# Kernel tuning notes

Measured on AMD Instinct MI355X. Metric: run time of the kernel, lower is better.

Reference implementation:

```python
import jax, jax.numpy as jnp
import numpy as np

N, C = 50000, 256
H, D = 8, 64          # num_heads, out_channels (per-head dim)
M = 64                # nb_random_features
EPS = 1e-6


def _create_projection_matrix(m, d, seed=0):
    """Performer orthogonal random features: stacked orthogonal blocks scaled by chi-norms."""
    rng = np.random.RandomState(seed)
    blocks = []
    nb_full = m // d
    for _ in range(nb_full):
        q, _ = np.linalg.qr(rng.randn(d, d))
        blocks.append(q.T)
    rem = m - nb_full * d
    if rem > 0:
        q, _ = np.linalg.qr(rng.randn(d, d))
        blocks.append(q.T[:rem])
    multiplier = np.linalg.norm(rng.randn(m, d), axis=1)  # scaling == 0 path
    return (multiplier[:, None] * np.vstack(blocks)).astype(np.float32)


def setup_inputs() -> dict:
    key = jax.random.key(0)
    ks = jax.random.split(key, 9)
    s = 0.05  # small init so exp() of random features stays well-conditioned
    return {
        "x":     jax.random.normal(ks[0], (N, C), dtype=jnp.float32),
        "Wq_w":  jax.random.normal(ks[1], (C, H * D), dtype=jnp.float32) * s,
        "Wq_b":  jnp.zeros((H * D,), dtype=jnp.float32),
        "Wk_w":  jax.random.normal(ks[2], (C, H * D), dtype=jnp.float32) * s,
        "Wk_b":  jnp.zeros((H * D,), dtype=jnp.float32),
        "Wv_w":  jax.random.normal(ks[3], (C, H * D), dtype=jnp.float32) * s,
        "Wv_b":  jnp.zeros((H * D,), dtype=jnp.float32),
        "Wo_w":  jax.random.normal(ks[4], (H * D, D), dtype=jnp.float32) * s,
        "Wo_b":  jnp.zeros((D,), dtype=jnp.float32),
        "proj":  jnp.asarray(_create_projection_matrix(M, D, seed=0)),  # [M, D]
    }


def _softmax_kernel(data, proj):
    # data: [B,N,H,D], proj: [M,D]
    data_normalizer = 1.0 / jnp.sqrt(jnp.sqrt(jnp.float32(data.shape[-1])))
    ratio = 1.0 / jnp.sqrt(jnp.float32(proj.shape[0]))
    data_dash = ratio * jnp.einsum("bnhd,md->bnhm", data_normalizer * data, proj)
    return jnp.exp(data_dash) + EPS


def reference(x, Wq_w, Wq_b, Wk_w, Wk_b, Wv_w, Wv_b, Wo_w, Wo_b, proj):
    xb = x[None]  # [1, N, C]
    B, n, _ = xb.shape
    Q = (xb @ Wq_w + Wq_b).reshape(B, n, H, D)
    K = (xb @ Wk_w + Wk_b).reshape(B, n, H, D)
    V = (xb @ Wv_w + Wv_b).reshape(B, n, H, D)

    Qp = _softmax_kernel(Q, proj)  # [B,N,H,M]
    Kp = _softmax_kernel(K, proj)  # [B,N,H,M]

    KV = jnp.einsum("bnhm,bnhd->bhmd", Kp, V)          # [B,H,M,D]
    Z_num = jnp.einsum("bnhm,bhmd->bnhd", Qp, KV)      # [B,N,H,D]
    Kp_sum = jnp.sum(Kp, axis=1)                        # [B,H,M]
    Z_den = jnp.einsum("bnhm,bhm->bnh", Qp, Kp_sum)[..., None]
    Z = (Z_num / (Z_den + EPS)).reshape(B, n, H * D)
    out = Z @ Wo_w + Wo_b                               # [B,N,D]
    return out[0]                                       # squeeze batch -> [N,D]
```

## Files before the change

kernel.cpp:

```cpp
#include <hip/hip_runtime.h>


#define NN      50000
#define HDIM    512
#define EPSF    1e-6f
#define SCALE   0.044194173824159224f
#define NCHK    196
#define KSLICE  28
#define NOUT    391
#define WP      264
#define TP      72
#define LDPB    36

typedef __bf16 bf16;
typedef __bf16 bf16x4 __attribute__((ext_vector_type(4)));
typedef __bf16 bf16x8 __attribute__((ext_vector_type(8)));
typedef float  f32x4  __attribute__((ext_vector_type(4)));

#define MFMA(a, b, c) __builtin_amdgcn_mfma_f32_16x16x32_bf16((a), (b), (c), 0, 0, 0)

__device__ __forceinline__ void lds_fence() {
    asm volatile("s_waitcnt lgkmcnt(0)" ::: "memory");
}

__global__ void prepx_kernel(const float* __restrict__ x, bf16* __restrict__ xb,
                             const float* __restrict__ Wq, const float* __restrict__ bq,
                             const float* __restrict__ Wk, const float* __restrict__ bk,
                             const float* __restrict__ Wv, const float* __restrict__ Wo,
                             const float* __restrict__ proj,
                             bf16* __restrict__ WqpT, bf16* __restrict__ WkpT,
                             bf16* __restrict__ WvT, bf16* __restrict__ WoT,
                             float* __restrict__ fqb, float* __restrict__ fkb)
{
    if (blockIdx.x < 2048) {
        for (int i8 = blockIdx.x * 256 + threadIdx.x; i8 < NN * 256 / 8;
             i8 += 2048 * 256) {
            const float4 a = reinterpret_cast<const float4*>(x)[i8 * 2];
            const float4 b = reinterpret_cast<const float4*>(x)[i8 * 2 + 1];
            bf16x8 r;
            r[0] = (bf16)a.x; r[1] = (bf16)a.y; r[2] = (bf16)a.z; r[3] = (bf16)a.w;
            r[4] = (bf16)b.x; r[5] = (bf16)b.y; r[6] = (bf16)b.z; r[7] = (bf16)b.w;
            reinterpret_cast<bf16x8*>(xb)[i8] = r;
        }
        return;
    }
    const int t = (blockIdx.x - 2048) * 256 + threadIdx.x;
    if (t < 131072) {
        const int row = t >> 8, c = t & 255;
        const int hh = row >> 6, m = row & 63;
        const float* pr = proj + m * 64;
        const float* wq = Wq + (size_t)c * HDIM + hh * 64;
        const float* wk = Wk + (size_t)c * HDIM + hh * 64;
        float sq = 0.f, sk = 0.f;
        for (int d = 0; d < 64; ++d) { const float p = pr[d]; sq += wq[d] * p; sk += wk[d] * p; }
        WqpT[(size_t)row * 256 + c] = (bf16)sq;
        WkpT[(size_t)row * 256 + c] = (bf16)sk;
    } else if (t < 262144) {
        const int i = t - 131072;
        const int col = i >> 8, c = i & 255;
        WvT[i] = (bf16)Wv[(size_t)c * HDIM + col];
    } else if (t < 262144 + 32768) {
        const int i = t - 262144;
        const int j = i >> 9, dp = i & 511;
        WoT[i] = (bf16)Wo[(size_t)dp * 64 + j];
    } else if (t < 262144 + 32768 + 1024) {
        const int i = t - 262144 - 32768;
        const int which = i >> 9, row = i & 511;
        const int hh = row >> 6, m = row & 63;
        const float* pr = proj + m * 64;
        const float* b = (which ? bk : bq) + hh * 64;
        float s = 0.f;
        for (int d = 0; d < 64; ++d) s += b[d] * pr[d];
        (which ? fkb : fqb)[row] = s;
    }
}

__global__ __launch_bounds__(512)
void kv_kernel(const bf16* __restrict__ xb,
               const bf16* __restrict__ WkpT, const float* __restrict__ fkb,
               const bf16* __restrict__ WvT,  const float* __restrict__ bv,
               float* __restrict__ pKV, float* __restrict__ pSum)
{
    __shared__ __align__(16) bf16 wk_lds[64 * WP];
    __shared__ __align__(16) bf16 wv_lds[64 * WP];
    __shared__ __align__(16) bf16 bufs[8][2][64 * LDPB];

    const int t     = threadIdx.x;
    const int w     = t >> 6;
    const int l     = t & 63;
    const int lr    = l & 15;
    const int lk    = l >> 4;
    const int slice = blockIdx.x;
    const int hd    = blockIdx.y;

    for (int i = t; i < 2048; i += 512) {
        const int row = i >> 5, c8 = i & 31;
        *reinterpret_cast<bf16x8*>(&wk_lds[row * WP + c8 * 8]) =
            *reinterpret_cast<const bf16x8*>(&WkpT[(size_t)(hd * 64 + row) * 256 + c8 * 8]);
        *reinterpret_cast<bf16x8*>(&wv_lds[row * WP + c8 * 8]) =
            *reinterpret_cast<const bf16x8*>(&WvT[(size_t)(hd * 64 + row) * 256 + c8 * 8]);
    }

    bf16* kptbuf = bufs[w][0];
    bf16* vtbuf  = bufs[w][1];

    f32x4 kvacc[16];
#pragma unroll
    for (int i = 0; i < 16; ++i) kvacc[i] = (f32x4){0.f, 0.f, 0.f, 0.f};
    float ksum_acc[4] = {0.f, 0.f, 0.f, 0.f};

    float fkbc[4], bvc[4];
#pragma unroll
    for (int q = 0; q < 4; ++q) {
        fkbc[q] = fkb[hd * 64 + q * 16 + lr];
        bvc [q] = bv [hd * 64 + q * 16 + lr];
    }
    __syncthreads();

    for (int chunk = slice; chunk < NCHK; chunk += KSLICE) {
        const int nbase = chunk * 256 + w * 32;

        lds_fence();

#pragma unroll
        for (int rt = 0; rt < 2; ++rt) {
            const bf16* xr = xb + (size_t)min(nbase + rt * 16 + lr, NN - 1) * 256;
            f32x4 fK[4];
#pragma unroll
            for (int q = 0; q < 4; ++q)
                fK[q] = (f32x4){fkbc[q], fkbc[q], fkbc[q], fkbc[q]};
#pragma unroll
            for (int kk = 0; kk < 8; ++kk) {
                const int off = kk * 32 + lk * 8;
                const bf16x8 xa = *reinterpret_cast<const bf16x8*>(xr + off);
#pragma unroll
                for (int mt = 0; mt < 4; ++mt) {
                    const bf16x8 wb = *reinterpret_cast<const bf16x8*>(
                        &wk_lds[(mt * 16 + lr) * WP + off]);
                    fK[mt] = MFMA(xa, wb, fK[mt]);
                }
            }
#pragma unroll
            for (int q = 0; q < 4; ++q) {
                bf16x4 kp4;
#pragma unroll
                for (int r = 0; r < 4; ++r) {
                    const int nl = rt * 16 + lk * 4 + r;
                    const float kpv = ((nbase + nl) < NN)
                                          ? (__expf(SCALE * fK[q][r]) + EPSF) : 0.f;
                    ksum_acc[q] += kpv;
                    kp4[r] = (bf16)kpv;
                }
                *reinterpret_cast<bf16x4*>(
                    &kptbuf[(q * 16 + lr) * LDPB + rt * 16 + lk * 4]) = kp4;
            }
        }

#pragma unroll
        for (int rt = 0; rt < 2; ++rt) {
            const bf16* xr = xb + (size_t)min(nbase + rt * 16 + lr, NN - 1) * 256;
            f32x4 aV[4];
#pragma unroll
            for (int q = 0; q < 4; ++q)
                aV[q] = (f32x4){bvc[q], bvc[q], bvc[q], bvc[q]};
#pragma unroll
            for (int kk = 0; kk < 8; ++kk) {
                const int off = kk * 32 + lk * 8;
                const bf16x8 xa = *reinterpret_cast<const bf16x8*>(xr + off);
#pragma unroll
                for (int dt = 0; dt < 4; ++dt) {
                    const bf16x8 wb = *reinterpret_cast<const bf16x8*>(
                        &wv_lds[(dt * 16 + lr) * WP + off]);
                    aV[dt] = MFMA(xa, wb, aV[dt]);
                }
            }
#pragma unroll
            for (int q = 0; q < 4; ++q) {
                bf16x4 vv4;
#pragma unroll
                for (int r = 0; r < 4; ++r) {
                    const int nl = rt * 16 + lk * 4 + r;
                    vv4[r] = ((nbase + nl) < NN) ? (bf16)aV[q][r] : (bf16)0.f;
                }
                *reinterpret_cast<bf16x4*>(
                    &vtbuf[(q * 16 + lr) * LDPB + rt * 16 + lk * 4]) = vv4;
            }
        }
        lds_fence();

        bf16x8 kpa[4], vb[4];
#pragma unroll
        for (int mt = 0; mt < 4; ++mt)
            kpa[mt] = *reinterpret_cast<const bf16x8*>(
                &kptbuf[(mt * 16 + lr) * LDPB + lk * 8]);
#pragma unroll
        for (int dt = 0; dt < 4; ++dt)
            vb[dt] = *reinterpret_cast<const bf16x8*>(
                &vtbuf[(dt * 16 + lr) * LDPB + lk * 8]);
#pragma unroll
        for (int mt = 0; mt < 4; ++mt)
#pragma unroll
            for (int dt = 0; dt < 4; ++dt)
                kvacc[mt * 4 + dt] = MFMA(kpa[mt], vb[dt], kvacc[mt * 4 + dt]);
    }

#pragma unroll
    for (int q = 0; q < 4; ++q) {
        float s = ksum_acc[q];
        s += __shfl_xor(s, 16, 64);
        s += __shfl_xor(s, 32, 64);
        ksum_acc[q] = s;
    }
    float* red  = (float*)(&bufs[0][0][0]);
    float* reds = red + 4096;

    __syncthreads();
    for (int i = 0; i < 8; ++i) {
        if (w == i) {
#pragma unroll
            for (int mt = 0; mt < 4; ++mt)
#pragma unroll
                for (int dt = 0; dt < 4; ++dt)
#pragma unroll
                    for (int r = 0; r < 4; ++r) {
                        const int md = (mt * 16 + lk * 4 + r) * 64 + dt * 16 + lr;
                        if (i == 0) red[md] = kvacc[mt * 4 + dt][r];
                        else        red[md] += kvacc[mt * 4 + dt][r];
                    }
            if (lk == 0) {
#pragma unroll
                for (int q = 0; q < 4; ++q) {
                    if (i == 0) reds[q * 16 + lr] = ksum_acc[q];
                    else        reds[q * 16 + lr] += ksum_acc[q];
                }
            }
        }
        __syncthreads();
    }
    float* dst = pKV + ((size_t)hd * KSLICE + slice) * 4096;
    for (int i = t; i < 4096; i += 512) dst[i] = red[i];
    if (t < 64) pSum[((size_t)hd * KSLICE + slice) * 64 + t] = reds[t];
}

__global__ void reduce_kernel(const float* __restrict__ pKV, const float* __restrict__ pSum,
                              bf16* __restrict__ KVT, float* __restrict__ Ksum)
{
    const int idx = blockIdx.x * 256 + threadIdx.x;
    if (idx < 8 * 4096) {
        const int h = idx >> 12, md = idx & 4095;
        const int m = md >> 6, d = md & 63;
        float s = 0.f;
        for (int b = 0; b < KSLICE; ++b) s += pKV[((size_t)h * KSLICE + b) * 4096 + md];
        KVT[h * 4096 + d * 64 + m] = (bf16)s;
    } else if (idx < 8 * 4096 + 512) {
        const int j = idx - 8 * 4096;
        const int h = j >> 6, m = j & 63;
        float s = 0.f;
        for (int b = 0; b < KSLICE; ++b) s += pSum[((size_t)h * KSLICE + b) * 64 + m];
        Ksum[j] = s;
    }
}

__global__ __launch_bounds__(512)
void out_kernel(const bf16* __restrict__ xb,
                const bf16* __restrict__ WqpT, const float* __restrict__ fqb,
                const bf16* __restrict__ KVT, const float* __restrict__ Ksum,
                const bf16* __restrict__ WoT, const float* __restrict__ bo,
                float* __restrict__ out)
{
    __shared__ __align__(16) bf16 wq_lds[64 * WP];
    __shared__ __align__(16) bf16 kvt_lds[64 * TP];
    __shared__ __align__(16) bf16 wo_lds[64 * TP];
    __shared__ __align__(16) bf16 tbufs[8][16 * TP];

    const int t  = threadIdx.x;
    const int w  = t >> 6;
    const int l  = t & 63;
    const int lr = l & 15;
    const int lk = l >> 4;
    bf16* tbuf = tbufs[w];
    const int nbase = blockIdx.x * 128 + w * 16;

    const bf16* xr = xb + (size_t)min(nbase + lr, NN - 1) * 256;
    bf16x8 xa[8];
#pragma unroll
    for (int kk = 0; kk < 8; ++kk)
        xa[kk] = *reinterpret_cast<const bf16x8*>(xr + kk * 32 + lk * 8);

    f32x4 oacc[4];
#pragma unroll
    for (int jt = 0; jt < 4; ++jt) {
        const float b = bo[jt * 16 + lr];
        oacc[jt] = (f32x4){b, b, b, b};
    }

    for (int h = 0; h < 8; ++h) {
        __syncthreads();
        for (int i = t; i < 2048; i += 512) {
            const int row = i >> 5, c8 = i & 31;
            *reinterpret_cast<bf16x8*>(&wq_lds[row * WP + c8 * 8]) =
                *reinterpret_cast<const bf16x8*>(&WqpT[(size_t)(h * 64 + row) * 256 + c8 * 8]);
        }
        {
            const int row = t >> 3, c8 = t & 7;
            *reinterpret_cast<bf16x8*>(&kvt_lds[row * TP + c8 * 8]) =
                *reinterpret_cast<const bf16x8*>(&KVT[h * 4096 + row * 64 + c8 * 8]);
            *reinterpret_cast<bf16x8*>(&wo_lds[row * TP + c8 * 8]) =
                *reinterpret_cast<const bf16x8*>(&WoT[(size_t)row * HDIM + h * 64 + c8 * 8]);
        }
        __syncthreads();

        f32x4 fQ[4];
#pragma unroll
        for (int mt = 0; mt < 4; ++mt) {
            const float b = fqb[h * 64 + mt * 16 + lr];
            fQ[mt] = (f32x4){b, b, b, b};
        }
#pragma unroll
        for (int kk = 0; kk < 8; ++kk) {
            const int off = kk * 32 + lk * 8;
#pragma unroll
            for (int mt = 0; mt < 4; ++mt) {
                const bf16x8 wb = *reinterpret_cast<const bf16x8*>(
                    &wq_lds[(mt * 16 + lr) * WP + off]);
                fQ[mt] = MFMA(xa[kk], wb, fQ[mt]);
            }
        }

        lds_fence();
        float denp[4] = {0.f, 0.f, 0.f, 0.f};
#pragma unroll
        for (int mt = 0; mt < 4; ++mt) {
            const float ks = Ksum[h * 64 + mt * 16 + lr];
#pragma unroll
            for (int r = 0; r < 4; ++r) {
                const float qp = __expf(SCALE * fQ[mt][r]) + EPSF;
                denp[r] += qp * ks;
                tbuf[(lk * 4 + r) * TP + mt * 16 + lr] = (bf16)qp;
            }
        }
#pragma unroll
        for (int r = 0; r < 4; ++r) {
            float s = denp[r];
            s += __shfl_xor(s, 1, 64);
            s += __shfl_xor(s, 2, 64);
            s += __shfl_xor(s, 4, 64);
            s += __shfl_xor(s, 8, 64);
            denp[r] = s;
        }
        lds_fence();

        bf16x8 qpa[2];
#pragma unroll
        for (int kk = 0; kk < 2; ++kk)
            qpa[kk] = *reinterpret_cast<const bf16x8*>(
                &tbuf[lr * TP + kk * 32 + lk * 8]);
        f32x4 num[4];
#pragma unroll
        for (int dt = 0; dt < 4; ++dt) num[dt] = (f32x4){0.f, 0.f, 0.f, 0.f};
#pragma unroll
        for (int dt = 0; dt < 4; ++dt)
#pragma unroll
            for (int kk = 0; kk < 2; ++kk) {
                const bf16x8 kvb = *reinterpret_cast<const bf16x8*>(
                    &kvt_lds[(dt * 16 + lr) * TP + kk * 32 + lk * 8]);
                num[dt] = MFMA(qpa[kk], kvb, num[dt]);
            }

        lds_fence();
#pragma unroll
        for (int dt = 0; dt < 4; ++dt)
#pragma unroll
            for (int r = 0; r < 4; ++r)
                tbuf[(lk * 4 + r) * TP + dt * 16 + lr] =
                    (bf16)(num[dt][r] / (denp[r] + EPSF));
        lds_fence();

        bf16x8 za[2];
#pragma unroll
        for (int kk = 0; kk < 2; ++kk)
            za[kk] = *reinterpret_cast<const bf16x8*>(
                &tbuf[lr * TP + kk * 32 + lk * 8]);
#pragma unroll
        for (int jt = 0; jt < 4; ++jt)
#pragma unroll
            for (int kk = 0; kk < 2; ++kk) {
                const bf16x8 wo = *reinterpret_cast<const bf16x8*>(
                    &wo_lds[(jt * 16 + lr) * TP + kk * 32 + lk * 8]);
                oacc[jt] = MFMA(za[kk], wo, oacc[jt]);
            }
    }

#pragma unroll
    for (int jt = 0; jt < 4; ++jt)
#pragma unroll
        for (int r = 0; r < 4; ++r) {
            const int n = nbase + lk * 4 + r;
            if (n < NN) out[(size_t)n * 64 + jt * 16 + lr] = oacc[jt][r];
        }
}

extern "C" void kernel_launch(void* const* d_in, const int* in_sizes, int n_in,
                              void* d_out, int out_size, void* d_ws, size_t ws_size,
                              hipStream_t stream) {
    const float* x    = (const float*)d_in[0];
    const float* Wq   = (const float*)d_in[1];
    const float* bq   = (const float*)d_in[2];
    const float* Wk   = (const float*)d_in[3];
    const float* bk   = (const float*)d_in[4];
    const float* Wv   = (const float*)d_in[5];
    const float* bv   = (const float*)d_in[6];
    const float* Wo   = (const float*)d_in[7];
    const float* bo   = (const float*)d_in[8];
    const float* proj = (const float*)d_in[9];
    float* out = (float*)d_out;

    char* ws = (char*)d_ws;
    float* Ksum = (float*)(ws + 0);
    float* fqb  = (float*)(ws + 2048);
    float* fkb  = (float*)(ws + 4096);
    bf16*  WqpT = (bf16*)(ws + 6144);
    bf16*  WkpT = (bf16*)(ws + 268288);
    bf16*  WvT  = (bf16*)(ws + 530432);
    bf16*  WoT  = (bf16*)(ws + 792576);
    bf16*  KVT  = (bf16*)(ws + 858112);
    bf16*  xb   = (bf16*)(ws + 923648);
    float* pKV  = (float*)(ws + 26523648);
    float* pSum = (float*)(ws + 30193664);

    prepx_kernel<<<dim3(2048 + 1156), 256, 0, stream>>>(
        x, xb, Wq, bq, Wk, bk, Wv, Wo, proj, WqpT, WkpT, WvT, WoT, fqb, fkb);
    kv_kernel<<<dim3(KSLICE, 8), 512, 0, stream>>>(xb, WkpT, fkb, WvT, bv, pKV, pSum);
    reduce_kernel<<<dim3(130), 256, 0, stream>>>(pKV, pSum, KVT, Ksum);
    out_kernel<<<dim3(NOUT), 512, 0, stream>>>(xb, WqpT, fqb, KVT, Ksum,
                                               WoT, bo, out);
}
```

Before: 160.8 us.

## Process two 16-row tiles per wave to reuse LDS weight fragments

In kv_kernel, the two row tiles per wave are now computed together so each LDS weight fragment load feeds two MFMAs instead of one. In out_kernel, blocks shrink to 256 threads with each wave handling 32 rows (two tiles), halving LDS weight reads per row. The x rows are reloaded from global memory per head instead of being held in registers. This raises register pressure and halves the number of waves per block in the output kernel, which may reduce latency hiding.

```diff
diff --git a/kernel.cpp b/kernel.cpp
--- a/kernel.cpp
+++ b/kernel.cpp
@@ -119,72 +119,82 @@
 
     for (int chunk = slice; chunk < NCHK; chunk += KSLICE) {
         const int nbase = chunk * 256 + w * 32;
+        const bf16* xr0 = xb + (size_t)min(nbase + lr,      NN - 1) * 256;
+        const bf16* xr1 = xb + (size_t)min(nbase + 16 + lr, NN - 1) * 256;
 
         lds_fence();
 
-#pragma unroll
-        for (int rt = 0; rt < 2; ++rt) {
-            const bf16* xr = xb + (size_t)min(nbase + rt * 16 + lr, NN - 1) * 256;
-            f32x4 fK[4];
-#pragma unroll
-            for (int q = 0; q < 4; ++q)
-                fK[q] = (f32x4){fkbc[q], fkbc[q], fkbc[q], fkbc[q]};
+        {
+            f32x4 fK[2][4];
+#pragma unroll
+            for (int q = 0; q < 4; ++q) {
+                fK[0][q] = (f32x4){fkbc[q], fkbc[q], fkbc[q], fkbc[q]};
+                fK[1][q] = fK[0][q];
+            }
 #pragma unroll
             for (int kk = 0; kk < 8; ++kk) {
                 const int off = kk * 32 + lk * 8;
-                const bf16x8 xa = *reinterpret_cast<const bf16x8*>(xr + off);
+                const bf16x8 xa0 = *reinterpret_cast<const bf16x8*>(xr0 + off);
+                const bf16x8 xa1 = *reinterpret_cast<const bf16x8*>(xr1 + off);
 #pragma unroll
                 for (int mt = 0; mt < 4; ++mt) {
                     const bf16x8 wb = *reinterpret_cast<const bf16x8*>(
                         &wk_lds[(mt * 16 + lr) * WP + off]);
-                    fK[mt] = MFMA(xa, wb, fK[mt]);
-                }
-            }
+                    fK[0][mt] = MFMA(xa0, wb, fK[0][mt]);
+                    fK[1][mt] = MFMA(xa1, wb, fK[1][mt]);
+                }
+            }
+#pragma unroll
+            for (int rt = 0; rt < 2; ++rt)
+#pragma unroll
+                for (int q = 0; q < 4; ++q) {
+                    bf16x4 kp4;
+#pragma unroll
+                    for (int r = 0; r < 4; ++r) {
+                        const int nl = rt * 16 + lk * 4 + r;
+                        const float kpv = ((nbase + nl) < NN)
+                                              ? (__expf(SCALE * fK[rt][q][r]) + EPSF) : 0.f;
+                        ksum_acc[q] += kpv;
+                        kp4[r] = (bf16)kpv;
+                    }
+                    *reinterpret_cast<bf16x4*>(
+                        &kptbuf[(q * 16 + lr) * LDPB + rt * 16 + lk * 4]) = kp4;
+                }
+        }
+
+        {
+            f32x4 aV[2][4];
 #pragma unroll
             for (int q = 0; q < 4; ++q) {
-                bf16x4 kp4;
-#pragma unroll
-                for (int r = 0; r < 4; ++r) {
-                    const int nl = rt * 16 + lk * 4 + r;
-                    const float kpv = ((nbase + nl) < NN)
-                                          ? (__expf(SCALE * fK[q][r]) + EPSF) : 0.f;
-                    ksum_acc[q] += kpv;
-                    kp4[r] = (bf16)kpv;
-                }
-                *reinterpret_cast<bf16x4*>(
-                    &kptbuf[(q * 16 + lr) * LDPB + rt * 16 + lk * 4]) = kp4;
-            }
-        }
-
-#pragma unroll
-        for (int rt = 0; rt < 2; ++rt) {
-            const bf16* xr = xb + (size_t)min(nbase + rt * 16 + lr, NN - 1) * 256;
-            f32x4 aV[4];
-#pragma unroll
-            for (int q = 0; q < 4; ++q)
-                aV[q] = (f32x4){bvc[q], bvc[q], bvc[q], bvc[q]};
+                aV[0][q] = (f32x4){bvc[q], bvc[q], bvc[q], bvc[q]};
+                aV[1][q] = aV[0][q];
+            }
 #pragma unroll
             for (int kk = 0; kk < 8; ++kk) {
                 const int off = kk * 32 + lk * 8;
-                const bf16x8 xa = *reinterpret_cast<const bf16x8*>(xr + off);
+                const bf16x8 xa0 = *reinterpret_cast<const bf16x8*>(xr0 + off);
+                const bf16x8 xa1 = *reinterpret_cast<const bf16x8*>(xr1 + off);
 #pragma unroll
                 for (int dt = 0; dt < 4; ++dt) {
                     const bf16x8 wb = *reinterpret_cast<const bf16x8*>(
                         &wv_lds[(dt * 16 + lr) * WP + off]);
-                    aV[dt] = MFMA(xa, wb, aV[dt]);
-                }
-            }
-#pragma unroll
-            for (int q = 0; q < 4; ++q) {
-                bf16x4 vv4;
-#pragma unroll
-                for (int r = 0; r < 4; ++r) {
-                    const int nl = rt * 16 + lk * 4 + r;
-                    vv4[r] = ((nbase + nl) < NN) ? (bf16)aV[q][r] : (bf16)0.f;
-                }
-                *reinterpret_cast<bf16x4*>(
-                    &vtbuf[(q * 16 + lr) * LDPB + rt * 16 + lk * 4]) = vv4;
-            }
+                    aV[0][dt] = MFMA(xa0, wb, aV[0][dt]);
+                    aV[1][dt] = MFMA(xa1, wb, aV[1][dt]);
+                }
+            }
+#pragma unroll
+            for (int rt = 0; rt < 2; ++rt)
+#pragma unroll
+                for (int q = 0; q < 4; ++q) {
+                    bf16x4 vv4;
+#pragma unroll
+                    for (int r = 0; r < 4; ++r) {
+                        const int nl = rt * 16 + lk * 4 + r;
+                        vv4[r] = ((nbase + nl) < NN) ? (bf16)aV[rt][q][r] : (bf16)0.f;
+                    }
+                    *reinterpret_cast<bf16x4*>(
+                        &vtbuf[(q * 16 + lr) * LDPB + rt * 16 + lk * 4]) = vv4;
+                }
         }
         lds_fence();
 
@@ -261,7 +271,7 @@
     }
 }
 
-__global__ __launch_bounds__(512)
+__global__ __launch_bounds__(256)
 void out_kernel(const bf16* __restrict__ xb,
                 const bf16* __restrict__ WqpT, const float* __restrict__ fqb,
                 const bf16* __restrict__ KVT, const float* __restrict__ Ksum,
@@ -271,7 +281,7 @@
     __shared__ __align__(16) bf16 wq_lds[64 * WP];
     __shared__ __align__(16) bf16 kvt_lds[64 * TP];
     __shared__ __align__(16) bf16 wo_lds[64 * TP];
-    __shared__ __align__(16) bf16 tbufs[8][16 * TP];
+    __shared__ __align__(16) bf16 tbufs[4][32 * TP];
 
     const int t  = threadIdx.x;
     const int w  = t >> 6;
@@ -279,30 +289,28 @@
     const int lr = l & 15;
     const int lk = l >> 4;
     bf16* tbuf = tbufs[w];
-    const int nbase = blockIdx.x * 128 + w * 16;
-
-    const bf16* xr = xb + (size_t)min(nbase + lr, NN - 1) * 256;
-    bf16x8 xa[8];
-#pragma unroll
-    for (int kk = 0; kk < 8; ++kk)
-        xa[kk] = *reinterpret_cast<const bf16x8*>(xr + kk * 32 + lk * 8);
-
-    f32x4 oacc[4];
+    const int nbase = blockIdx.x * 128 + w * 32;
+
+    const bf16* xr0 = xb + (size_t)min(nbase + lr,      NN - 1) * 256;
+    const bf16* xr1 = xb + (size_t)min(nbase + 16 + lr, NN - 1) * 256;
+
+    f32x4 oacc[2][4];
 #pragma unroll
     for (int jt = 0; jt < 4; ++jt) {
         const float b = bo[jt * 16 + lr];
-        oacc[jt] = (f32x4){b, b, b, b};
+        oacc[0][jt] = (f32x4){b, b, b, b};
+        oacc[1][jt] = oacc[0][jt];
     }
 
     for (int h = 0; h < 8; ++h) {
         __syncthreads();
-        for (int i = t; i < 2048; i += 512) {
+        for (int i = t; i < 2048; i += 256) {
             const int row = i >> 5, c8 = i & 31;
             *reinterpret_cast<bf16x8*>(&wq_lds[row * WP + c8 * 8]) =
                 *reinterpret_cast<const bf16x8*>(&WqpT[(size_t)(h * 64 + row) * 256 + c8 * 8]);
         }
-        {
-            const int row = t >> 3, c8 = t & 7;
+        for (int i = t; i < 512; i += 256) {
+            const int row = i >> 3, c8 = i & 7;
             *reinterpret_cast<bf16x8*>(&kvt_lds[row * TP + c8 * 8]) =
                 *reinterpret_cast<const bf16x8*>(&KVT[h * 4096 + row * 64 + c8 * 8]);
             *reinterpret_cast<bf16x8*>(&wo_lds[row * TP + c8 * 8]) =
@@ -310,94 +318,114 @@
         }
         __syncthreads();
 
-        f32x4 fQ[4];
+        f32x4 fQ[2][4];
 #pragma unroll
         for (int mt = 0; mt < 4; ++mt) {
             const float b = fqb[h * 64 + mt * 16 + lr];
-            fQ[mt] = (f32x4){b, b, b, b};
+            fQ[0][mt] = (f32x4){b, b, b, b};
+            fQ[1][mt] = fQ[0][mt];
         }
 #pragma unroll
         for (int kk = 0; kk < 8; ++kk) {
             const int off = kk * 32 + lk * 8;
+            const bf16x8 xa0 = *reinterpret_cast<const bf16x8*>(xr0 + off);
+            const bf16x8 xa1 = *reinterpret_cast<const bf16x8*>(xr1 + off);
 #pragma unroll
             for (int mt = 0; mt < 4; ++mt) {
                 const bf16x8 wb = *reinterpret_cast<const bf16x8*>(
                     &wq_lds[(mt * 16 + lr) * WP + off]);
-                fQ[mt] = MFMA(xa[kk], wb, fQ[mt]);
-            }
-        }
-
+                fQ[0][mt] = MFMA(xa0, wb, fQ[0][mt]);
+                fQ[1][mt] = MFMA(xa1, wb, fQ[1][mt]);
+            }
+        }
+
+        float denp[2][4] = {{0.f,0.f,0.f,0.f},{0.f,0.f,0.f,0.f}};
+#pragma unroll
+        for (int rt = 0; rt < 2; ++rt)
+#pragma unroll
+            for (int mt = 0; mt < 4; ++mt) {
+                const float ks = Ksum[h * 64 + mt * 16 + lr];
+#pragma unroll
+                for (int r = 0; r < 4; ++r) {
+                    const float qp = __expf(SCALE * fQ[rt][mt][r]) + EPSF;
+                    denp[rt][r] += qp * ks;
+                    tbuf[(rt * 16 + lk * 4 + r) * TP + mt * 16 + lr] = (bf16)qp;
+                }
+            }
+#pragma unroll
+        for (int rt = 0; rt < 2; ++rt)
+#pragma unroll
+            for (int r = 0; r < 4; ++r) {
+                float s = denp[rt][r];
+                s += __shfl_xor(s, 1, 64);
+                s += __shfl_xor(s, 2, 64);
+                s += __shfl_xor(s, 4, 64);
+                s += __shfl_xor(s, 8, 64);
+                denp[rt][r] = s;
+            }
         lds_fence();
-        float denp[4] = {0.f, 0.f, 0.f, 0.f};
-#pragma unroll
-        for (int mt = 0; mt < 4; ++mt) {
-            const float ks = Ksum[h * 64 + mt * 16 + lr];
-#pragma unroll
-            for (int r = 0; r < 4; ++r) {
-                const float qp = __expf(SCALE * fQ[mt][r]) + EPSF;
-                denp[r] += qp * ks;
-                tbuf[(lk * 4 + r) * TP + mt * 16 + lr] = (bf16)qp;
-            }
-        }
-#pragma unroll
-        for (int r = 0; r < 4; ++r) {
-            float s = denp[r];
-            s += __shfl_xor(s, 1, 64);
-            s += __shfl_xor(s, 2, 64);
-            s += __shfl_xor(s, 4, 64);
-            s += __shfl_xor(s, 8, 64);
-            denp[r] = s;
-        }
-        lds_fence();
-
-        bf16x8 qpa[2];
-#pragma unroll
-        for (int kk = 0; kk < 2; ++kk)
-            qpa[kk] = *reinterpret_cast<const bf16x8*>(
-                &tbuf[lr * TP + kk * 32 + lk * 8]);
-        f32x4 num[4];
-#pragma unroll
-        for (int dt = 0; dt < 4; ++dt) num[dt] = (f32x4){0.f, 0.f, 0.f, 0.f};
+
+        bf16x8 qpa[2][2];
+#pragma unroll
+        for (int rt = 0; rt < 2; ++rt)
+#pragma unroll
+            for (int kk = 0; kk < 2; ++kk)
+                qpa[rt][kk] = *reinterpret_cast<const bf16x8*>(
+                    &tbuf[(rt * 16 + lr) * TP + kk * 32 + lk * 8]);
+        f32x4 num[2][4];
+#pragma unroll
+        for (int dt = 0; dt < 4; ++dt) {
+            num[0][dt] = (f32x4){0.f, 0.f, 0.f, 0.f};
+            num[1][dt] = num[0][dt];
+        }
 #pragma unroll
         for (int dt = 0; dt < 4; ++dt)
 #pragma unroll
             for (int kk = 0; kk < 2; ++kk) {
                 const bf16x8 kvb = *reinterpret_cast<const bf16x8*>(
                     &kvt_lds[(dt * 16 + lr) * TP + kk * 32 + lk * 8]);
-                num[dt] = MFMA(qpa[kk], kvb, num[dt]);
+                num[0][dt] = MFMA(qpa[0][kk], kvb, num[0][dt]);
+                num[1][dt] = MFMA(qpa[1][kk], kvb, num[1][dt]);
             }
 
         lds_fence();
 #pragma unroll
-        for (int dt = 0; dt < 4; ++dt)
-#pragma unroll
-            for (int r = 0; r < 4; ++r)
-                tbuf[(lk * 4 + r) * TP + dt * 16 + lr] =
-                    (bf16)(num[dt][r] / (denp[r] + EPSF));
+        for (int rt = 0; rt < 2; ++rt)
+#pragma unroll
+            for (int dt = 0; dt < 4; ++dt)
+#pragma unroll
+                for (int r = 0; r < 4; ++r)
+                    tbuf[(rt * 16 + lk * 4 + r) * TP + dt * 16 + lr] =
+                        (bf16)(num[rt][dt][r] / (denp[rt][r] + EPSF));
         lds_fence();
 
-        bf16x8 za[2];
-#pragma unroll
-        for (int kk = 0; kk < 2; ++kk)
-            za[kk] = *reinterpret_cast<const bf16x8*>(
-                &tbuf[lr * TP + kk * 32 + lk * 8]);
+        bf16x8 za[2][2];
+#pragma unroll
+        for (int rt = 0; rt < 2; ++rt)
+#pragma unroll
+            for (int kk = 0; kk < 2; ++kk)
+                za[rt][kk] = *reinterpret_cast<const bf16x8*>(
+                    &tbuf[(rt * 16 + lr) * TP + kk * 32 + lk * 8]);
 #pragma unroll
         for (int jt = 0; jt < 4; ++jt)
 #pragma unroll
             for (int kk = 0; kk < 2; ++kk) {
                 const bf16x8 wo = *reinterpret_cast<const bf16x8*>(
                     &wo_lds[(jt * 16 + lr) * TP + kk * 32 + lk * 8]);
-                oacc[jt] = MFMA(za[kk], wo, oacc[jt]);
-            }
-    }
-
-#pragma unroll
-    for (int jt = 0; jt < 4; ++jt)
-#pragma unroll
-        for (int r = 0; r < 4; ++r) {
-            const int n = nbase + lk * 4 + r;
-            if (n < NN) out[(size_t)n * 64 + jt * 16 + lr] = oacc[jt][r];
-        }
+                oacc[0][jt] = MFMA(za[0][kk], wo, oacc[0][jt]);
+                oacc[1][jt] = MFMA(za[1][kk], wo, oacc[1][jt]);
+            }
+    }
+
+#pragma unroll
+    for (int rt = 0; rt < 2; ++rt)
+#pragma unroll
+        for (int jt = 0; jt < 4; ++jt)
+#pragma unroll
+            for (int r = 0; r < 4; ++r) {
+                const int n = nbase + rt * 16 + lk * 4 + r;
+                if (n < NN) out[(size_t)n * 64 + jt * 16 + lr] = oacc[rt][jt][r];
+            }
 }
 
 extern "C" void kernel_launch(void* const* d_in, const int* in_sizes, int n_in,
@@ -432,6 +460,6 @@
         x, xb, Wq, bq, Wk, bk, Wv, Wo, proj, WqpT, WkpT, WvT, WoT, fqb, fkb);
     kv_kernel<<<dim3(KSLICE, 8), 512, 0, stream>>>(xb, WkpT, fkb, WvT, bv, pKV, pSum);
     reduce_kernel<<<dim3(130), 256, 0, stream>>>(pKV, pSum, KVT, Ksum);
-    out_kernel<<<dim3(NOUT), 512, 0, stream>>>(xb, WqpT, fqb, KVT, Ksum,
+    out_kernel<<<dim3(NOUT), 256, 0, stream>>>(xb, WqpT, fqb, KVT, Ksum,
                                                WoT, bo, out);
 }
```

Result: slower. 173.6 us (+8.0%).

## Interleave two row tiles in K/V projection; read out-kernel weights from global

Applied to the files above, without the earlier changes.

In the KV-accumulation kernel, the K and V projections now process both 16-row tiles together, so each LDS weight fragment is loaded once and used for two MFMAs. This roughly halves LDS weight traffic and gives independent MFMA chains more room to overlap, at the cost of more accumulator registers. In the output kernel, the per-head LDS staging of Wq, KV and Wo and both block barriers are removed, and the MFMAs read weight fragments straight from global memory (through cache). This drops barrier stalls and LDS use, which may allow higher occupancy, but risks more global and cache traffic.

```diff
diff --git a/kernel.cpp b/kernel.cpp
--- a/kernel.cpp
+++ b/kernel.cpp
@@ -119,72 +119,82 @@
 
     for (int chunk = slice; chunk < NCHK; chunk += KSLICE) {
         const int nbase = chunk * 256 + w * 32;
-
-        lds_fence();
-
-#pragma unroll
-        for (int rt = 0; rt < 2; ++rt) {
-            const bf16* xr = xb + (size_t)min(nbase + rt * 16 + lr, NN - 1) * 256;
-            f32x4 fK[4];
-#pragma unroll
-            for (int q = 0; q < 4; ++q)
-                fK[q] = (f32x4){fkbc[q], fkbc[q], fkbc[q], fkbc[q]};
+        const bf16* xr0 = xb + (size_t)min(nbase + lr,      NN - 1) * 256;
+        const bf16* xr1 = xb + (size_t)min(nbase + 16 + lr, NN - 1) * 256;
+
+        lds_fence();
+
+        {
+            f32x4 fK[2][4];
+#pragma unroll
+            for (int q = 0; q < 4; ++q) {
+                fK[0][q] = (f32x4){fkbc[q], fkbc[q], fkbc[q], fkbc[q]};
+                fK[1][q] = fK[0][q];
+            }
 #pragma unroll
             for (int kk = 0; kk < 8; ++kk) {
                 const int off = kk * 32 + lk * 8;
-                const bf16x8 xa = *reinterpret_cast<const bf16x8*>(xr + off);
+                const bf16x8 xa0 = *reinterpret_cast<const bf16x8*>(xr0 + off);
+                const bf16x8 xa1 = *reinterpret_cast<const bf16x8*>(xr1 + off);
 #pragma unroll
                 for (int mt = 0; mt < 4; ++mt) {
                     const bf16x8 wb = *reinterpret_cast<const bf16x8*>(
                         &wk_lds[(mt * 16 + lr) * WP + off]);
-                    fK[mt] = MFMA(xa, wb, fK[mt]);
+                    fK[0][mt] = MFMA(xa0, wb, fK[0][mt]);
+                    fK[1][mt] = MFMA(xa1, wb, fK[1][mt]);
                 }
             }
 #pragma unroll
+            for (int rt = 0; rt < 2; ++rt)
+#pragma unroll
+                for (int q = 0; q < 4; ++q) {
+                    bf16x4 kp4;
+#pragma unroll
+                    for (int r = 0; r < 4; ++r) {
+                        const int nl = rt * 16 + lk * 4 + r;
+                        const float kpv = ((nbase + nl) < NN)
+                                              ? (__expf(SCALE * fK[rt][q][r]) + EPSF) : 0.f;
+                        ksum_acc[q] += kpv;
+                        kp4[r] = (bf16)kpv;
+                    }
+                    *reinterpret_cast<bf16x4*>(
+                        &kptbuf[(q * 16 + lr) * LDPB + rt * 16 + lk * 4]) = kp4;
+                }
+        }
+
+        {
+            f32x4 aV[2][4];
+#pragma unroll
             for (int q = 0; q < 4; ++q) {
-                bf16x4 kp4;
-#pragma unroll
-                for (int r = 0; r < 4; ++r) {
-                    const int nl = rt * 16 + lk * 4 + r;
-                    const float kpv = ((nbase + nl) < NN)
-                                          ? (__expf(SCALE * fK[q][r]) + EPSF) : 0.f;
-                    ksum_acc[q] += kpv;
-                    kp4[r] = (bf16)kpv;
-                }
-                *reinterpret_cast<bf16x4*>(
-                    &kptbuf[(q * 16 + lr) * LDPB + rt * 16 + lk * 4]) = kp4;
-            }
-        }
-
-#pragma unroll
-        for (int rt = 0; rt < 2; ++rt) {
-            const bf16* xr = xb + (size_t)min(nbase + rt * 16 + lr, NN - 1) * 256;
-            f32x4 aV[4];
-#pragma unroll
-            for (int q = 0; q < 4; ++q)
-                aV[q] = (f32x4){bvc[q], bvc[q], bvc[q], bvc[q]};
+                aV[0][q] = (f32x4){bvc[q], bvc[q], bvc[q], bvc[q]};
+                aV[1][q] = aV[0][q];
+            }
 #pragma unroll
             for (int kk = 0; kk < 8; ++kk) {
                 const int off = kk * 32 + lk * 8;
-                const bf16x8 xa = *reinterpret_cast<const bf16x8*>(xr + off);
+                const bf16x8 xa0 = *reinterpret_cast<const bf16x8*>(xr0 + off);
+                const bf16x8 xa1 = *reinterpret_cast<const bf16x8*>(xr1 + off);
 #pragma unroll
                 for (int dt = 0; dt < 4; ++dt) {
                     const bf16x8 wb = *reinterpret_cast<const bf16x8*>(
                         &wv_lds[(dt * 16 + lr) * WP + off]);
-                    aV[dt] = MFMA(xa, wb, aV[dt]);
+                    aV[0][dt] = MFMA(xa0, wb, aV[0][dt]);
+                    aV[1][dt] = MFMA(xa1, wb, aV[1][dt]);
                 }
             }
 #pragma unroll
-            for (int q = 0; q < 4; ++q) {
-                bf16x4 vv4;
-#pragma unroll
-                for (int r = 0; r < 4; ++r) {
-                    const int nl = rt * 16 + lk * 4 + r;
-                    vv4[r] = ((nbase + nl) < NN) ? (bf16)aV[q][r] : (bf16)0.f;
+            for (int rt = 0; rt < 2; ++rt)
+#pragma unroll
+                for (int q = 0; q < 4; ++q) {
+                    bf16x4 vv4;
+#pragma unroll
+                    for (int r = 0; r < 4; ++r) {
+                        const int nl = rt * 16 + lk * 4 + r;
+                        vv4[r] = ((nbase + nl) < NN) ? (bf16)aV[rt][q][r] : (bf16)0.f;
+                    }
+                    *reinterpret_cast<bf16x4*>(
+                        &vtbuf[(q * 16 + lr) * LDPB + rt * 16 + lk * 4]) = vv4;
                 }
-                *reinterpret_cast<bf16x4*>(
-                    &vtbuf[(q * 16 + lr) * LDPB + rt * 16 + lk * 4]) = vv4;
-            }
         }
         lds_fence();
 
@@ -268,11 +278,7 @@
                 const bf16* __restrict__ WoT, const float* __restrict__ bo,
                 float* __restrict__ out)
 {
-    __shared__ __align__(16) bf16 wq_lds[64 * WP];
-    __shared__ __align__(16) bf16 kvt_lds[64 * TP];
-    __shared__ __align__(16) bf16 wo_lds[64 * TP];
     __shared__ __align__(16) bf16 tbufs[8][16 * TP];
-
     const int t  = threadIdx.x;
     const int w  = t >> 6;
     const int l  = t & 63;
@@ -295,21 +301,6 @@
     }
 
     for (int h = 0; h < 8; ++h) {
-        __syncthreads();
-        for (int i = t; i < 2048; i += 512) {
-            const int row = i >> 5, c8 = i & 31;
-            *reinterpret_cast<bf16x8*>(&wq_lds[row * WP + c8 * 8]) =
-                *reinterpret_cast<const bf16x8*>(&WqpT[(size_t)(h * 64 + row) * 256 + c8 * 8]);
-        }
-        {
-            const int row = t >> 3, c8 = t & 7;
-            *reinterpret_cast<bf16x8*>(&kvt_lds[row * TP + c8 * 8]) =
-                *reinterpret_cast<const bf16x8*>(&KVT[h * 4096 + row * 64 + c8 * 8]);
-            *reinterpret_cast<bf16x8*>(&wo_lds[row * TP + c8 * 8]) =
-                *reinterpret_cast<const bf16x8*>(&WoT[(size_t)row * HDIM + h * 64 + c8 * 8]);
-        }
-        __syncthreads();
-
         f32x4 fQ[4];
 #pragma unroll
         for (int mt = 0; mt < 4; ++mt) {
@@ -322,7 +313,7 @@
 #pragma unroll
             for (int mt = 0; mt < 4; ++mt) {
                 const bf16x8 wb = *reinterpret_cast<const bf16x8*>(
-                    &wq_lds[(mt * 16 + lr) * WP + off]);
+                    &WqpT[(size_t)(h * 64 + mt * 16 + lr) * 256 + off]);
                 fQ[mt] = MFMA(xa[kk], wb, fQ[mt]);
             }
         }
@@ -363,7 +354,7 @@
 #pragma unroll
             for (int kk = 0; kk < 2; ++kk) {
                 const bf16x8 kvb = *reinterpret_cast<const bf16x8*>(
-                    &kvt_lds[(dt * 16 + lr) * TP + kk * 32 + lk * 8]);
+                    &KVT[h * 4096 + (dt * 16 + lr) * 64 + kk * 32 + lk * 8]);
                 num[dt] = MFMA(qpa[kk], kvb, num[dt]);
             }
 
@@ -386,7 +377,7 @@
 #pragma unroll
             for (int kk = 0; kk < 2; ++kk) {
                 const bf16x8 wo = *reinterpret_cast<const bf16x8*>(
-                    &wo_lds[(jt * 16 + lr) * TP + kk * 32 + lk * 8]);
+                    &WoT[(size_t)(jt * 16 + lr) * HDIM + h * 64 + kk * 32 + lk * 8]);
                 oacc[jt] = MFMA(za[kk], wo, oacc[jt]);
             }
     }
```

New measurement: 310.5 us. 93.1% more time.

## Feed K-features and V directly from MFMA output registers into KV accumulation

Applied to the files above, without the earlier changes.

Fuses the K and V projection loops so each loaded x fragment feeds both weight matrices. The K-feature and V tiles are no longer staged through per-wave LDS transposition buffers. Instead, the 16x16 MFMA accumulator layout is reused directly as operands of a 16x16x16 bf16 MFMA issued via inline asm with a manual s_nop. The slice count rises from 28 to 64 to raise parallelism, with the pSum workspace offset moved and the reduction scratch reusing wk_lds. The risks are hazard handling in the inline asm, higher register pressure, and a larger partial-reduction workload.

```diff
diff --git a/kernel.cpp b/kernel.cpp
--- a/kernel.cpp
+++ b/kernel.cpp
@@ -6,11 +6,10 @@
 #define EPSF    1e-6f
 #define SCALE   0.044194173824159224f
 #define NCHK    196
-#define KSLICE  28
+#define KSLICE  64
 #define NOUT    391
 #define WP      264
 #define TP      72
-#define LDPB    36
 
 typedef __bf16 bf16;
 typedef __bf16 bf16x4 __attribute__((ext_vector_type(4)));
@@ -18,6 +17,12 @@
 typedef float  f32x4  __attribute__((ext_vector_type(4)));
 
 #define MFMA(a, b, c) __builtin_amdgcn_mfma_f32_16x16x32_bf16((a), (b), (c), 0, 0, 0)
+
+__device__ __forceinline__ f32x4 mfma16(bf16x4 a, bf16x4 b, f32x4 c) {
+    asm volatile("s_nop 1\n\tv_mfma_f32_16x16x16_bf16 %0, %1, %2, %0"
+                 : "+v"(c) : "v"(a), "v"(b));
+    return c;
+}
 
 __device__ __forceinline__ void lds_fence() {
     asm volatile("s_waitcnt lgkmcnt(0)" ::: "memory");
@@ -83,7 +88,6 @@
 {
     __shared__ __align__(16) bf16 wk_lds[64 * WP];
     __shared__ __align__(16) bf16 wv_lds[64 * WP];
-    __shared__ __align__(16) bf16 bufs[8][2][64 * LDPB];
 
     const int t     = threadIdx.x;
     const int w     = t >> 6;
@@ -101,9 +105,6 @@
             *reinterpret_cast<const bf16x8*>(&WvT[(size_t)(hd * 64 + row) * 256 + c8 * 8]);
     }
 
-    bf16* kptbuf = bufs[w][0];
-    bf16* vtbuf  = bufs[w][1];
-
     f32x4 kvacc[16];
 #pragma unroll
     for (int i = 0; i < 16; ++i) kvacc[i] = (f32x4){0.f, 0.f, 0.f, 0.f};
@@ -120,88 +121,54 @@
     for (int chunk = slice; chunk < NCHK; chunk += KSLICE) {
         const int nbase = chunk * 256 + w * 32;
 
-        lds_fence();
-
 #pragma unroll
         for (int rt = 0; rt < 2; ++rt) {
             const bf16* xr = xb + (size_t)min(nbase + rt * 16 + lr, NN - 1) * 256;
-            f32x4 fK[4];
-#pragma unroll
-            for (int q = 0; q < 4; ++q)
+
+            f32x4 fK[4], aV[4];
+#pragma unroll
+            for (int q = 0; q < 4; ++q) {
                 fK[q] = (f32x4){fkbc[q], fkbc[q], fkbc[q], fkbc[q]};
+                aV[q] = (f32x4){bvc[q], bvc[q], bvc[q], bvc[q]};
+            }
 #pragma unroll
             for (int kk = 0; kk < 8; ++kk) {
                 const int off = kk * 32 + lk * 8;
                 const bf16x8 xa = *reinterpret_cast<const bf16x8*>(xr + off);
 #pragma unroll
                 for (int mt = 0; mt < 4; ++mt) {
-                    const bf16x8 wb = *reinterpret_cast<const bf16x8*>(
+                    const bf16x8 wbk = *reinterpret_cast<const bf16x8*>(
                         &wk_lds[(mt * 16 + lr) * WP + off]);
-                    fK[mt] = MFMA(xa, wb, fK[mt]);
+                    fK[mt] = MFMA(xa, wbk, fK[mt]);
                 }
-            }
+#pragma unroll
+                for (int dt = 0; dt < 4; ++dt) {
+                    const bf16x8 wbv = *reinterpret_cast<const bf16x8*>(
+                        &wv_lds[(dt * 16 + lr) * WP + off]);
+                    aV[dt] = MFMA(xa, wbv, aV[dt]);
+                }
+            }
+
+            bf16x4 kp16[4], vv16[4];
 #pragma unroll
             for (int q = 0; q < 4; ++q) {
-                bf16x4 kp4;
 #pragma unroll
                 for (int r = 0; r < 4; ++r) {
                     const int nl = rt * 16 + lk * 4 + r;
-                    const float kpv = ((nbase + nl) < NN)
-                                          ? (__expf(SCALE * fK[q][r]) + EPSF) : 0.f;
+                    const bool valid = (nbase + nl) < NN;
+                    const float kpv = valid ? (__expf(SCALE * fK[q][r]) + EPSF) : 0.f;
                     ksum_acc[q] += kpv;
-                    kp4[r] = (bf16)kpv;
+                    kp16[q][r] = (bf16)kpv;
+                    vv16[q][r] = valid ? (bf16)aV[q][r] : (bf16)0.f;
                 }
-                *reinterpret_cast<bf16x4*>(
-                    &kptbuf[(q * 16 + lr) * LDPB + rt * 16 + lk * 4]) = kp4;
-            }
-        }
-
-#pragma unroll
-        for (int rt = 0; rt < 2; ++rt) {
-            const bf16* xr = xb + (size_t)min(nbase + rt * 16 + lr, NN - 1) * 256;
-            f32x4 aV[4];
-#pragma unroll
-            for (int q = 0; q < 4; ++q)
-                aV[q] = (f32x4){bvc[q], bvc[q], bvc[q], bvc[q]};
-#pragma unroll
-            for (int kk = 0; kk < 8; ++kk) {
-                const int off = kk * 32 + lk * 8;
-                const bf16x8 xa = *reinterpret_cast<const bf16x8*>(xr + off);
-#pragma unroll
-                for (int dt = 0; dt < 4; ++dt) {
-                    const bf16x8 wb = *reinterpret_cast<const bf16x8*>(
-                        &wv_lds[(dt * 16 + lr) * WP + off]);
-                    aV[dt] = MFMA(xa, wb, aV[dt]);
-                }
-            }
-#pragma unroll
-            for (int q = 0; q < 4; ++q) {
-                bf16x4 vv4;
-#pragma unroll
-                for (int r = 0; r < 4; ++r) {
-                    const int nl = rt * 16 + lk * 4 + r;
-                    vv4[r] = ((nbase + nl) < NN) ? (bf16)aV[q][r] : (bf16)0.f;
-                }
-                *reinterpret_cast<bf16x4*>(
-                    &vtbuf[(q * 16 + lr) * LDPB + rt * 16 + lk * 4]) = vv4;
-            }
-        }
-        lds_fence();
-
-        bf16x8 kpa[4], vb[4];
-#pragma unroll
-        for (int mt = 0; mt < 4; ++mt)
-            kpa[mt] = *reinterpret_cast<const bf16x8*>(
-                &kptbuf[(mt * 16 + lr) * LDPB + lk * 8]);
-#pragma unroll
-        for (int dt = 0; dt < 4; ++dt)
-            vb[dt] = *reinterpret_cast<const bf16x8*>(
-                &vtbuf[(dt * 16 + lr) * LDPB + lk * 8]);
-#pragma unroll
-        for (int mt = 0; mt < 4; ++mt)
-#pragma unroll
-            for (int dt = 0; dt < 4; ++dt)
-                kvacc[mt * 4 + dt] = MFMA(kpa[mt], vb[dt], kvacc[mt * 4 + dt]);
+            }
+
+#pragma unroll
+            for (int mt = 0; mt < 4; ++mt)
+#pragma unroll
+                for (int dt = 0; dt < 4; ++dt)
+                    kvacc[mt * 4 + dt] = mfma16(kp16[mt], vv16[dt], kvacc[mt * 4 + dt]);
+        }
     }
 
 #pragma unroll
@@ -211,7 +178,7 @@
         s += __shfl_xor(s, 32, 64);
         ksum_acc[q] = s;
     }
-    float* red  = (float*)(&bufs[0][0][0]);
+    float* red  = (float*)wk_lds;
     float* reds = red + 4096;
 
     __syncthreads();
@@ -426,7 +393,7 @@
     bf16*  KVT  = (bf16*)(ws + 858112);
     bf16*  xb   = (bf16*)(ws + 923648);
     float* pKV  = (float*)(ws + 26523648);
-    float* pSum = (float*)(ws + 30193664);
+    float* pSum = (float*)(ws + 34912256);
 
     prepx_kernel<<<dim3(2048 + 1156), 256, 0, stream>>>(
         x, xb, Wq, bq, Wk, bk, Wv, Wo, proj, WqpT, WkpT, WvT, WoT, fqb, fkb);
```

After: 169.6 us. +5.5%, slower.
